# Kernel tuning notes

Hardware: AMD Instinct MI355X
Metric: run time of the kernel (lower is better)

The kernel has to match this reference:

```python
import jax, jax.numpy as jnp
import numpy as np

E, N, D, H, K, S = 800000, 50000, 96, 8, 12, 32  # edges, nodes, dim, heads, head_dim, edge_scalar_dim


def smooth_leaky_relu(x, a=0.2):
    # equiformer SmoothLeakyReLU: (1+a)/2 * x + (1-a)/2 * x * (2*sigmoid(x) - 1)
    return ((1 + a) / 2) * x + ((1 - a) / 2) * x * (2 * jax.nn.sigmoid(x) - 1)


def setup_inputs() -> dict:
    key = jax.random.key(0)
    ks = jax.random.split(key, 16)
    inv = lambda n: 1.0 / np.sqrt(n)
    return {
        "message": jax.random.normal(ks[0], (E, D), jnp.float32),
        "edge_attr": jax.random.normal(ks[1], (E, 1), jnp.float32),
        "edge_scalars": jax.random.normal(ks[2], (E, S), jnp.float32),
        "W_rad1": jax.random.normal(ks[3], (S, S), jnp.float32) * inv(S),
        "b_rad1": jnp.zeros((S,), jnp.float32),
        "W_rad2": jax.random.normal(ks[4], (S, D), jnp.float32) * inv(S),
        "b_rad2": jnp.zeros((D,), jnp.float32),
        "W_alpha": jax.random.normal(ks[5], (D, D), jnp.float32) * inv(D),
        "W_lin": jax.random.normal(ks[6], (D, D), jnp.float32) * inv(D),
        "w_dtp2": jax.random.normal(ks[7], (D,), jnp.float32),
        "W_lin2": jax.random.normal(ks[8], (D, D), jnp.float32) * inv(D),
        "alpha_dot": jax.random.normal(ks[9], (H, K), jnp.float32) * inv(K),
        "W_proj": jax.random.normal(ks[10], (D, D), jnp.float32) * inv(D),
        "edge_dst": jnp.sort(jax.random.randint(ks[11], (E,), 0, N)),
        "n_nodes_dst": N,
    }


def reference(message, edge_attr, edge_scalars, W_rad1, b_rad1, W_rad2, b_rad2,
              W_alpha, W_lin, w_dtp2, W_lin2, alpha_dot, W_proj,
              edge_dst, n_nodes_dst):
    # sep_act.dtp_rad: radial MLP on edge scalars -> depthwise TP weights [E, D]
    weight = jax.nn.silu(edge_scalars @ W_rad1 + b_rad1) @ W_rad2 + b_rad2
    # sep_act.dtp: depthwise tensor product (scalar irreps -> per-channel product)
    msg = message * edge_attr * weight                      # [E, D]
    # sep_alpha: LinearRS to mul_alpha scalars, split into heads
    log_alpha = (msg @ W_alpha).reshape(E, H, K)            # [E, H, K]
    # sep_act.lin + gate (scalar gate == SiLU)
    value = jax.nn.silu(msg @ W_lin)                        # [E, D]
    # sep_value: internal-weight depthwise TP + linear
    value = (value * edge_attr * w_dtp2) @ W_lin2           # [E, D]
    # attention logits
    la = smooth_leaky_relu(log_alpha)
    logits = jnp.einsum('ehk,hk->eh', la, alpha_dot)        # [E, H]
    # scatter_logsumexp over destination nodes (segment softmax)
    m = jax.ops.segment_max(logits, edge_dst, num_segments=n_nodes_dst)     # [N, H]
    z = jax.ops.segment_sum(jnp.exp(logits - m[edge_dst]), edge_dst,
                            num_segments=n_nodes_dst)
    log_Z = m + jnp.log(z)                                  # [N, H]
    alpha = jnp.exp(logits - log_Z[edge_dst])               # [E, H]
    # weighted scatter-sum aggregation
    attn = jax.ops.segment_sum(value.reshape(E, H, K) * alpha[:, :, None],
                               edge_dst, num_segments=n_nodes_dst)          # [N, H, K]
    # heads2vec + proj
    return attn.reshape(n_nodes_dst, D) @ W_proj            # [N, D]
```

## Files before the change

kernel.cpp:

```cpp
#include <hip/hip_runtime.h>
#include <hip/hip_bf16.h>
#include <math.h>

#define D 96
#define H 8
#define KH 12
#define S 32

typedef __attribute__((ext_vector_type(8))) short short8;
typedef __attribute__((ext_vector_type(4))) float f32x4;

#define MFMA(a, b, c) __builtin_amdgcn_mfma_f32_16x16x32_bf16(a, b, c, 0, 0, 0)

__device__ __forceinline__ float sigmoidf_(float x) { return 1.0f / (1.0f + __expf(-x)); }
__device__ __forceinline__ float siluf_(float x) { return x * sigmoidf_(x); }
__device__ __forceinline__ float slrelu_(float x) {
    float s = sigmoidf_(x);
    return 0.6f * x + 0.4f * x * (2.0f * s - 1.0f);
}
__device__ __forceinline__ short f2bf(float f) {
    unsigned int u = __float_as_uint(f);
    u += 0x7fffu + ((u >> 16) & 1u);
    return (short)(u >> 16);
}
__device__ __forceinline__ float bf2f(ushort u) {
    return __uint_as_float(((unsigned int)u) << 16);
}

__global__ void pack_weights_kernel(
    const float* __restrict__ W1, const float* __restrict__ W2,
    const float* __restrict__ WA, const float* __restrict__ WL,
    const float* __restrict__ WL2, short* __restrict__ wB)
{
    int tid = blockIdx.x * 256 + threadIdx.x;
    if (tid >= 62 * 512) return;
    int j    = tid & 7;
    int lane = (tid >> 3) & 63;
    int fi   = tid >> 9;
    int q = lane >> 4, ln = lane & 15;
    const float* src; int ncols, tt, ff;
    if (fi < 2)       { src = W1;  ncols = 32; tt = fi;            ff = 0; }
    else if (fi < 8)  { src = W2;  ncols = 96; tt = fi - 2;        ff = 0; }
    else if (fi < 26) { src = WA;  ncols = 96; tt = (fi - 8) / 3;  ff = (fi - 8) % 3; }
    else if (fi < 44) { src = WL;  ncols = 96; tt = (fi - 26) / 3; ff = (fi - 26) % 3; }
    else              { src = WL2; ncols = 96; tt = (fi - 44) / 3; ff = (fi - 44) % 3; }
    int k = ff * 32 + q * 8 + j;
    int n = tt * 16 + ln;
    wB[tid] = f2bf(src[k * ncols + n]);
}

__global__ __launch_bounds__(256) void rowptr_kernel(
    const int* __restrict__ dst, int* __restrict__ rp, int E, int N)
{
    int e = blockIdx.x * 256 + threadIdx.x;
    if (e >= E) return;
    int cur  = dst[e];
    int prev = (e == 0) ? -1 : dst[e - 1];
    for (int n = prev + 1; n <= cur; n++) rp[n] = e;
    if (e == E - 1)
        for (int n = cur + 1; n <= N; n++) rp[n] = E;
}

__global__ __launch_bounds__(256, 6) void fused_edge_kernel(
    const float* __restrict__ message, const float* __restrict__ ea,
    const float* __restrict__ xs,
    const float* __restrict__ b1, const float* __restrict__ b2,
    const float* __restrict__ wdtp2, const float* __restrict__ adot,
    const short* __restrict__ wB,
    ushort* __restrict__ value, float* __restrict__ logits, int E)
{
    __shared__ __align__(16) char uni[64 * 97 * 4];
    short* sB = (short*)uni;
    float* sS = (float*)uni;
    const short8* wB8 = (const short8*)wB;

    const int t    = threadIdx.x;
    const int lane = t & 63;
    const int w    = t >> 6;
    const int q    = lane >> 4;
    const int ln   = lane & 15;
    const int row0 = blockIdx.x * 64;

    const int mA = w * 16 + ln;
    const int gA = row0 + mA;
    const int mC = w * 16 + q * 4;

    short8 af;
    {
        float4 x0 = make_float4(0, 0, 0, 0), x1 = x0;
        if (gA < E) {
            const float4* p = (const float4*)&xs[(size_t)gA * S + q * 8];
            x0 = p[0]; x1 = p[1];
        }
        af[0] = f2bf(x0.x); af[1] = f2bf(x0.y); af[2] = f2bf(x0.z); af[3] = f2bf(x0.w);
        af[4] = f2bf(x1.x); af[5] = f2bf(x1.y); af[6] = f2bf(x1.z); af[7] = f2bf(x1.w);
    }
    {
        f32x4 h0 = {0, 0, 0, 0}, h1 = {0, 0, 0, 0};
        h0 = MFMA(af, wB8[0 * 64 + lane], h0);
        h1 = MFMA(af, wB8[1 * 64 + lane], h1);
#pragma unroll
        for (int r = 0; r < 4; r++) {
            sB[(mC + r) * 104 + ln]      = f2bf(siluf_(h0[r] + b1[ln]));
            sB[(mC + r) * 104 + 16 + ln] = f2bf(siluf_(h1[r] + b1[16 + ln]));
        }
    }

    f32x4 acc[6];
    {
        short8 hf = *(const short8*)&sB[mA * 104 + q * 8];
#pragma unroll
        for (int i = 0; i < 6; i++) acc[i] = (f32x4){0, 0, 0, 0};
#pragma unroll
        for (int i = 0; i < 6; i++) acc[i] = MFMA(hf, wB8[(2 + i) * 64 + lane], acc[i]);
    }
    float eaR[4];
#pragma unroll
    for (int r = 0; r < 4; r++) {
        int gm = row0 + mC + r;
        eaR[r] = (gm < E) ? ea[gm] : 0.0f;
    }
#pragma unroll
    for (int i = 0; i < 6; i++) {
        int n = i * 16 + ln;
#pragma unroll
        for (int r = 0; r < 4; r++) {
            int gm = row0 + mC + r;
            float mv = (gm < E) ? message[(size_t)gm * D + n] : 0.0f;
            sB[(mC + r) * 104 + n] = f2bf(mv * eaR[r] * (acc[i][r] + b2[n]));
        }
    }

    short8 mf0 = *(const short8*)&sB[mA * 104 + 0  + q * 8];
    short8 mf1 = *(const short8*)&sB[mA * 104 + 32 + q * 8];
    short8 mf2 = *(const short8*)&sB[mA * 104 + 64 + q * 8];
    __syncthreads();

#pragma unroll
    for (int i = 0; i < 6; i++) acc[i] = (f32x4){0, 0, 0, 0};
#pragma unroll
    for (int i = 0; i < 6; i++) {
        acc[i] = MFMA(mf0, wB8[(8 + i * 3 + 0) * 64 + lane], acc[i]);
        acc[i] = MFMA(mf1, wB8[(8 + i * 3 + 1) * 64 + lane], acc[i]);
        acc[i] = MFMA(mf2, wB8[(8 + i * 3 + 2) * 64 + lane], acc[i]);
    }
#pragma unroll
    for (int i = 0; i < 6; i++) {
        int n = i * 16 + ln;
#pragma unroll
        for (int r = 0; r < 4; r++)
            sS[(mC + r) * 97 + n] = slrelu_(acc[i][r]);
    }
    __syncthreads();
    {
        int e = t & 63;
        int gm = row0 + e;
#pragma unroll
        for (int hh = 0; hh < 2; hh++) {
            int h = (t >> 6) * 2 + hh;
            float lg = 0.0f;
#pragma unroll
            for (int k = 0; k < KH; k++)
                lg += sS[e * 97 + h * KH + k] * adot[h * KH + k];
            if (gm < E) logits[(size_t)gm * H + h] = lg;
        }
    }
    __syncthreads();

#pragma unroll
    for (int i = 0; i < 6; i++) acc[i] = (f32x4){0, 0, 0, 0};
#pragma unroll
    for (int i = 0; i < 6; i++) {
        acc[i] = MFMA(mf0, wB8[(26 + i * 3 + 0) * 64 + lane], acc[i]);
        acc[i] = MFMA(mf1, wB8[(26 + i * 3 + 1) * 64 + lane], acc[i]);
        acc[i] = MFMA(mf2, wB8[(26 + i * 3 + 2) * 64 + lane], acc[i]);
    }
#pragma unroll
    for (int i = 0; i < 6; i++) {
        int n = i * 16 + ln;
#pragma unroll
        for (int r = 0; r < 4; r++)
            sB[(mC + r) * 104 + n] = f2bf(siluf_(acc[i][r]) * eaR[r] * wdtp2[n]);
    }

    {
        short8 vf0 = *(const short8*)&sB[mA * 104 + 0  + q * 8];
        short8 vf1 = *(const short8*)&sB[mA * 104 + 32 + q * 8];
        short8 vf2 = *(const short8*)&sB[mA * 104 + 64 + q * 8];
#pragma unroll
        for (int i = 0; i < 6; i++) acc[i] = (f32x4){0, 0, 0, 0};
#pragma unroll
        for (int i = 0; i < 6; i++) {
            acc[i] = MFMA(vf0, wB8[(44 + i * 3 + 0) * 64 + lane], acc[i]);
            acc[i] = MFMA(vf1, wB8[(44 + i * 3 + 1) * 64 + lane], acc[i]);
            acc[i] = MFMA(vf2, wB8[(44 + i * 3 + 2) * 64 + lane], acc[i]);
        }
#pragma unroll
        for (int i = 0; i < 6; i++) {
            int n = i * 16 + ln;
#pragma unroll
            for (int r = 0; r < 4; r++) {
                int gm = row0 + mC + r;
                if (gm < E) value[(size_t)gm * D + n] = (ushort)f2bf(acc[i][r]);
            }
        }
    }
}

__global__ __launch_bounds__(256) void logz_alpha_kernel(
    const float* __restrict__ logits, const int* __restrict__ rp,
    float* __restrict__ alpha, int N)
{
    int tid = blockIdx.x * 256 + threadIdx.x;
    if (tid >= N * H) return;
    int n = tid >> 3, h = tid & 7;
    int s = rp[n], e1 = rp[n + 1];
    if (s >= e1) return;
    float m = -INFINITY;
    for (int e = s; e < e1; e++) m = fmaxf(m, logits[(size_t)e * H + h]);
    float z = 0.0f;
    for (int e = s; e < e1; e++) {
        float a = __expf(logits[(size_t)e * H + h] - m);
        z += a;
        alpha[(size_t)e * H + h] = a;
    }
    float inv = 1.0f / z;
    for (int e = s; e < e1; e++) alpha[(size_t)e * H + h] *= inv;
}

__global__ __launch_bounds__(256) void aggregate_kernel(
    const ushort* __restrict__ value, const float* __restrict__ alpha,
    const int* __restrict__ rp, float* __restrict__ attn, int N)
{
    int tid = blockIdx.x * 256 + threadIdx.x;
    if (tid >= N * D) return;
    int n = tid / D, d = tid % D;
    int h = d / KH;
    int s = rp[n], e1 = rp[n + 1];
    float acc = 0.0f;
    for (int e = s; e < e1; e++)
        acc += bf2f(value[(size_t)e * D + d]) * alpha[(size_t)e * H + h];
    attn[tid] = acc;
}

__global__ __launch_bounds__(192) void gemm96_out_kernel(
    const float* __restrict__ src, const float* __restrict__ W,
    float* __restrict__ dst, int rows)
{
    __shared__ float sW[D * D];
    __shared__ float tile[64 * (D + 1)];

    const int t = threadIdx.x;
    const int row0 = blockIdx.x * 64;

    for (int i = t; i < D * D; i += 192) sW[i] = W[i];
    for (int i = t; i < 64 * D; i += 192) {
        int e = i / D, d = i % D;
        int r = row0 + e;
        tile[e * (D + 1) + d] = (r < rows) ? src[(size_t)r * D + d] : 0.0f;
    }
    __syncthreads();

    const int e0 = (t & 15) * 4;
    const int d0 = (t >> 4) * 8;

    float acc[4][8];
#pragma unroll
    for (int a = 0; a < 4; a++)
#pragma unroll
        for (int j = 0; j < 8; j++) acc[a][j] = 0.0f;

    for (int kk = 0; kk < D; kk++) {
        float4 w0 = *(const float4*)&sW[kk * D + d0];
        float4 w1 = *(const float4*)&sW[kk * D + d0 + 4];
#pragma unroll
        for (int a = 0; a < 4; a++) {
            float m = tile[(e0 + a) * (D + 1) + kk];
            acc[a][0] += m * w0.x; acc[a][1] += m * w0.y;
            acc[a][2] += m * w0.z; acc[a][3] += m * w0.w;
            acc[a][4] += m * w1.x; acc[a][5] += m * w1.y;
            acc[a][6] += m * w1.z; acc[a][7] += m * w1.w;
        }
    }
#pragma unroll
    for (int a = 0; a < 4; a++) {
        int r = row0 + e0 + a;
        if (r >= rows) continue;
        *(float4*)&dst[(size_t)r * D + d0]     = make_float4(acc[a][0], acc[a][1], acc[a][2], acc[a][3]);
        *(float4*)&dst[(size_t)r * D + d0 + 4] = make_float4(acc[a][4], acc[a][5], acc[a][6], acc[a][7]);
    }
}

extern "C" void kernel_launch(void* const* d_in, const int* in_sizes, int n_in,
                              void* d_out, int out_size, void* d_ws, size_t ws_size,
                              hipStream_t stream)
{
    const float* message      = (const float*)d_in[0];
    const float* edge_attr    = (const float*)d_in[1];
    const float* edge_scalars = (const float*)d_in[2];
    const float* W_rad1       = (const float*)d_in[3];
    const float* b_rad1       = (const float*)d_in[4];
    const float* W_rad2       = (const float*)d_in[5];
    const float* b_rad2       = (const float*)d_in[6];
    const float* W_alpha      = (const float*)d_in[7];
    const float* W_lin        = (const float*)d_in[8];
    const float* w_dtp2       = (const float*)d_in[9];
    const float* W_lin2       = (const float*)d_in[10];
    const float* alpha_dot    = (const float*)d_in[11];
    const float* W_proj       = (const float*)d_in[12];
    const int*   edge_dst     = (const int*)d_in[13];
    float* out = (float*)d_out;

    const int E = in_sizes[0] / D;
    const int N = out_size / D;

    char* ws = (char*)d_ws;
    ushort* value  = (ushort*)ws;
    float*  logits = (float*)(ws + (size_t)E * D * 2);
    float*  alphaB = (float*)((char*)logits + (size_t)E * H * 4);
    float*  attn   = (float*)((char*)alphaB + (size_t)E * H * 4);
    int*    rp     = (int*)((char*)attn + (size_t)N * D * 4);
    short*  wBuf   = (short*)((char*)rp + (size_t)(N + 1) * 4);

    pack_weights_kernel<<<(62 * 512 + 255) / 256, 256, 0, stream>>>(
        W_rad1, W_rad2, W_alpha, W_lin, W_lin2, wBuf);
    rowptr_kernel<<<(E + 255) / 256, 256, 0, stream>>>(edge_dst, rp, E, N);
    fused_edge_kernel<<<(E + 63) / 64, 256, 0, stream>>>(
        message, edge_attr, edge_scalars, b_rad1, b_rad2, w_dtp2, alpha_dot,
        wBuf, value, logits, E);
    logz_alpha_kernel<<<(N * H + 255) / 256, 256, 0, stream>>>(logits, rp, alphaB, N);
    aggregate_kernel<<<(N * D + 255) / 256, 256, 0, stream>>>(value, alphaB, rp, attn, N);
    gemm96_out_kernel<<<(N + 63) / 64, 192, 0, stream>>>(attn, W_proj, out, N);
}
```

Baseline: 876.1 us.

## Defer softmax normalization, vectorize aggregation, and use bf16 MFMA for output projection

The softmax normalization pass over alpha is removed. The unnormalized exponentials are kept along with a per-node inverse sum, and that inverse is applied once after aggregation. Aggregation now has each thread accumulate 4 bf16 channels through 8-byte loads and writes bf16 attention output. The fp32 LDS output GEMM is replaced by a bf16 MFMA projection kernel that uses prepacked W_proj fragments. This cuts edge-array traffic and the cost of the final GEMM, at the price of rounding the attention output to bf16 before projection.

Result: faster. 784.0 us (-10.5%).

```diff
diff --git a/kernel.cpp b/kernel.cpp
--- a/kernel.cpp
+++ b/kernel.cpp
@@ -30,10 +30,11 @@
 __global__ void pack_weights_kernel(
     const float* __restrict__ W1, const float* __restrict__ W2,
     const float* __restrict__ WA, const float* __restrict__ WL,
-    const float* __restrict__ WL2, short* __restrict__ wB)
+    const float* __restrict__ WL2, const float* __restrict__ WP,
+    short* __restrict__ wB)
 {
     int tid = blockIdx.x * 256 + threadIdx.x;
-    if (tid >= 62 * 512) return;
+    if (tid >= 80 * 512) return;
     int j    = tid & 7;
     int lane = (tid >> 3) & 63;
     int fi   = tid >> 9;
@@ -43,7 +44,8 @@
     else if (fi < 8)  { src = W2;  ncols = 96; tt = fi - 2;        ff = 0; }
     else if (fi < 26) { src = WA;  ncols = 96; tt = (fi - 8) / 3;  ff = (fi - 8) % 3; }
     else if (fi < 44) { src = WL;  ncols = 96; tt = (fi - 26) / 3; ff = (fi - 26) % 3; }
-    else              { src = WL2; ncols = 96; tt = (fi - 44) / 3; ff = (fi - 44) % 3; }
+    else if (fi < 62) { src = WL2; ncols = 96; tt = (fi - 44) / 3; ff = (fi - 44) % 3; }
+    else              { src = WP;  ncols = 96; tt = (fi - 62) / 3; ff = (fi - 62) % 3; }
     int k = ff * 32 + q * 8 + j;
     int n = tt * 16 + ln;
     wB[tid] = f2bf(src[k * ncols + n]);
@@ -209,85 +211,90 @@
 
 __global__ __launch_bounds__(256) void logz_alpha_kernel(
     const float* __restrict__ logits, const int* __restrict__ rp,
-    float* __restrict__ alpha, int N)
+    float* __restrict__ alphaU, float* __restrict__ zinv, int N)
 {
     int tid = blockIdx.x * 256 + threadIdx.x;
     if (tid >= N * H) return;
     int n = tid >> 3, h = tid & 7;
     int s = rp[n], e1 = rp[n + 1];
-    if (s >= e1) return;
     float m = -INFINITY;
     for (int e = s; e < e1; e++) m = fmaxf(m, logits[(size_t)e * H + h]);
     float z = 0.0f;
     for (int e = s; e < e1; e++) {
         float a = __expf(logits[(size_t)e * H + h] - m);
         z += a;
-        alpha[(size_t)e * H + h] = a;
-    }
-    float inv = 1.0f / z;
-    for (int e = s; e < e1; e++) alpha[(size_t)e * H + h] *= inv;
+        alphaU[(size_t)e * H + h] = a;
+    }
+    zinv[tid] = (z > 0.0f) ? (1.0f / z) : 0.0f;
 }
 
 __global__ __launch_bounds__(256) void aggregate_kernel(
-    const ushort* __restrict__ value, const float* __restrict__ alpha,
-    const int* __restrict__ rp, float* __restrict__ attn, int N)
+    const ushort* __restrict__ value, const float* __restrict__ alphaU,
+    const float* __restrict__ zinv, const int* __restrict__ rp,
+    ushort* __restrict__ attnB, int N)
 {
     int tid = blockIdx.x * 256 + threadIdx.x;
-    if (tid >= N * D) return;
-    int n = tid / D, d = tid % D;
-    int h = d / KH;
+    if (tid >= N * 24) return;
+    int n = tid / 24, g = tid % 24;
+    int d0 = g * 4, h = g / 3;
     int s = rp[n], e1 = rp[n + 1];
-    float acc = 0.0f;
-    for (int e = s; e < e1; e++)
-        acc += bf2f(value[(size_t)e * D + d]) * alpha[(size_t)e * H + h];
-    attn[tid] = acc;
-}
-
-__global__ __launch_bounds__(192) void gemm96_out_kernel(
-    const float* __restrict__ src, const float* __restrict__ W,
-    float* __restrict__ dst, int rows)
-{
-    __shared__ float sW[D * D];
-    __shared__ float tile[64 * (D + 1)];
-
-    const int t = threadIdx.x;
+    const char* vb = (const char*)value;
+    float a0 = 0.0f, a1 = 0.0f, a2 = 0.0f, a3 = 0.0f;
+    for (int e = s; e < e1; e++) {
+        uint2 v = *(const uint2*)(vb + (size_t)e * 192 + d0 * 2);
+        float a = alphaU[(size_t)e * H + h];
+        a0 += __uint_as_float(v.x << 16) * a;
+        a1 += __uint_as_float(v.x & 0xffff0000u) * a;
+        a2 += __uint_as_float(v.y << 16) * a;
+        a3 += __uint_as_float(v.y & 0xffff0000u) * a;
+    }
+    float zi = zinv[n * H + h];
+    ushort4 o;
+    o.x = (ushort)f2bf(a0 * zi);
+    o.y = (ushort)f2bf(a1 * zi);
+    o.z = (ushort)f2bf(a2 * zi);
+    o.w = (ushort)f2bf(a3 * zi);
+    *(ushort4*)&attnB[(size_t)n * D + d0] = o;
+}
+
+__global__ __launch_bounds__(256) void proj_kernel(
+    const ushort* __restrict__ attnB, const short* __restrict__ wB,
+    float* __restrict__ out, int rows)
+{
+    const short8* wB8 = (const short8*)wB;
+    const int t    = threadIdx.x;
+    const int lane = t & 63;
+    const int w    = t >> 6;
+    const int q    = lane >> 4;
+    const int ln   = lane & 15;
     const int row0 = blockIdx.x * 64;
-
-    for (int i = t; i < D * D; i += 192) sW[i] = W[i];
-    for (int i = t; i < 64 * D; i += 192) {
-        int e = i / D, d = i % D;
-        int r = row0 + e;
-        tile[e * (D + 1) + d] = (r < rows) ? src[(size_t)r * D + d] : 0.0f;
-    }
-    __syncthreads();
-
-    const int e0 = (t & 15) * 4;
-    const int d0 = (t >> 4) * 8;
-
-    float acc[4][8];
-#pragma unroll
-    for (int a = 0; a < 4; a++)
-#pragma unroll
-        for (int j = 0; j < 8; j++) acc[a][j] = 0.0f;
-
-    for (int kk = 0; kk < D; kk++) {
-        float4 w0 = *(const float4*)&sW[kk * D + d0];
-        float4 w1 = *(const float4*)&sW[kk * D + d0 + 4];
-#pragma unroll
-        for (int a = 0; a < 4; a++) {
-            float m = tile[(e0 + a) * (D + 1) + kk];
-            acc[a][0] += m * w0.x; acc[a][1] += m * w0.y;
-            acc[a][2] += m * w0.z; acc[a][3] += m * w0.w;
-            acc[a][4] += m * w1.x; acc[a][5] += m * w1.y;
-            acc[a][6] += m * w1.z; acc[a][7] += m * w1.w;
-        }
-    }
-#pragma unroll
-    for (int a = 0; a < 4; a++) {
-        int r = row0 + e0 + a;
-        if (r >= rows) continue;
-        *(float4*)&dst[(size_t)r * D + d0]     = make_float4(acc[a][0], acc[a][1], acc[a][2], acc[a][3]);
-        *(float4*)&dst[(size_t)r * D + d0 + 4] = make_float4(acc[a][4], acc[a][5], acc[a][6], acc[a][7]);
+    const int mA   = w * 16 + ln;
+    const int gA   = row0 + mA;
+    const int mC   = w * 16 + q * 4;
+
+    short8 mf0 = {0,0,0,0,0,0,0,0}, mf1 = mf0, mf2 = mf0;
+    if (gA < rows) {
+        mf0 = *(const short8*)&attnB[(size_t)gA * D + 0  + q * 8];
+        mf1 = *(const short8*)&attnB[(size_t)gA * D + 32 + q * 8];
+        mf2 = *(const short8*)&attnB[(size_t)gA * D + 64 + q * 8];
+    }
+    f32x4 acc[6];
+#pragma unroll
+    for (int i = 0; i < 6; i++) acc[i] = (f32x4){0, 0, 0, 0};
+#pragma unroll
+    for (int i = 0; i < 6; i++) {
+        acc[i] = MFMA(mf0, wB8[(62 + i * 3 + 0) * 64 + lane], acc[i]);
+        acc[i] = MFMA(mf1, wB8[(62 + i * 3 + 1) * 64 + lane], acc[i]);
+        acc[i] = MFMA(mf2, wB8[(62 + i * 3 + 2) * 64 + lane], acc[i]);
+    }
+#pragma unroll
+    for (int i = 0; i < 6; i++) {
+        int nn = i * 16 + ln;
+#pragma unroll
+        for (int r = 0; r < 4; r++) {
+            int gm = row0 + mC + r;
+            if (gm < rows) out[(size_t)gm * D + nn] = acc[i][r];
+        }
     }
 }
 
@@ -314,21 +321,22 @@
     const int E = in_sizes[0] / D;
     const int N = out_size / D;
 
-    char* ws = (char*)d_ws;
-    ushort* value  = (ushort*)ws;
-    float*  logits = (float*)(ws + (size_t)E * D * 2);
-    float*  alphaB = (float*)((char*)logits + (size_t)E * H * 4);
-    float*  attn   = (float*)((char*)alphaB + (size_t)E * H * 4);
-    int*    rp     = (int*)((char*)attn + (size_t)N * D * 4);
-    short*  wBuf   = (short*)((char*)rp + (size_t)(N + 1) * 4);
-
-    pack_weights_kernel<<<(62 * 512 + 255) / 256, 256, 0, stream>>>(
-        W_rad1, W_rad2, W_alpha, W_lin, W_lin2, wBuf);
+    char* p = (char*)d_ws;
+    ushort* value  = (ushort*)p;            p += (size_t)E * D * 2;
+    float*  logits = (float*)p;             p += (size_t)E * H * 4;
+    float*  alphaU = (float*)p;             p += (size_t)E * H * 4;
+    float*  zinv   = (float*)p;             p += (size_t)N * H * 4;
+    ushort* attnB  = (ushort*)p;            p += (size_t)N * D * 2;
+    int*    rp     = (int*)p;               p += ((size_t)(N + 1) * 4 + 15) & ~(size_t)15;
+    short*  wBuf   = (short*)p;
+
+    pack_weights_kernel<<<(80 * 512 + 255) / 256, 256, 0, stream>>>(
+        W_rad1, W_rad2, W_alpha, W_lin, W_lin2, W_proj, wBuf);
     rowptr_kernel<<<(E + 255) / 256, 256, 0, stream>>>(edge_dst, rp, E, N);
     fused_edge_kernel<<<(E + 63) / 64, 256, 0, stream>>>(
         message, edge_attr, edge_scalars, b_rad1, b_rad2, w_dtp2, alpha_dot,
         wBuf, value, logits, E);
-    logz_alpha_kernel<<<(N * H + 255) / 256, 256, 0, stream>>>(logits, rp, alphaB, N);
-    aggregate_kernel<<<(N * D + 255) / 256, 256, 0, stream>>>(value, alphaB, rp, attn, N);
-    gemm96_out_kernel<<<(N + 63) / 64, 192, 0, stream>>>(attn, W_proj, out, N);
-}
+    logz_alpha_kernel<<<(N * H + 255) / 256, 256, 0, stream>>>(logits, rp, alphaU, zinv, N);
+    aggregate_kernel<<<(N * 24 + 255) / 256, 256, 0, stream>>>(value, alphaU, zinv, rp, attnB, N);
+    proj_kernel<<<(N + 63) / 64, 256, 0, stream>>>(attnB, wBuf, out, N);
+}
```
